# Optimization experiments

Hardware: AMD Instinct MI355X
Metric: run time of the kernel (lower is better)

The kernel has to match this reference:

```python
import jax, jax.numpy as jnp
import numpy as np

D_MODEL = 1024
N_HEAD = 16
D_HEAD = D_MODEL // N_HEAD


def setup_inputs() -> dict:
    key = jax.random.key(0)
    k_x, k_wqkv, k_bqkv, k_wp, k_bp = jax.random.split(key, 5)
    B, T = 2, 2048
    bound = 1.0 / np.sqrt(D_MODEL)
    return {
        "x": jax.random.normal(k_x, (B, T, D_MODEL), dtype=jnp.float32),
        "w_qkv": jax.random.uniform(k_wqkv, (D_MODEL, 3 * D_MODEL), jnp.float32, -bound, bound),
        "b_qkv": jax.random.uniform(k_bqkv, (3 * D_MODEL,), jnp.float32, -bound, bound),
        "w_proj": jax.random.uniform(k_wp, (D_MODEL, D_MODEL), jnp.float32, -bound, bound),
        "b_proj": jax.random.uniform(k_bp, (D_MODEL,), jnp.float32, -bound, bound),
    }


def reference(x, w_qkv, b_qkv, w_proj, b_proj):
    B, T, C = x.shape
    qkv = x @ w_qkv + b_qkv                       # [B,T,3C]
    qkv = qkv.reshape(B, T, 3, N_HEAD, D_HEAD)
    qkv = jnp.transpose(qkv, (2, 0, 3, 1, 4))      # [3,B,H,T,dh]
    q, k, v = qkv[0], qkv[1], qkv[2]
    scale = np.sqrt(D_HEAD).astype(np.float32)
    attn = jnp.einsum("bhqd,bhkd->bhqk", q, k) / scale  # [B,H,T,T]
    causal = jnp.tril(jnp.ones((T, T), dtype=bool))
    attn = jnp.where(causal, attn, -jnp.inf)
    attn = jax.nn.softmax(attn, axis=-1)
    out = jnp.einsum("bhqk,bhkd->bhqd", attn, v)   # [B,H,T,dh]
    out = jnp.transpose(out, (0, 2, 1, 3)).reshape(B, T, C)
    return out @ w_proj + b_proj
```

## Files before the change

kernel.cpp:

```cpp
#include <hip/hip_runtime.h>
#include <hip/hip_bf16.h>
#include <math.h>

constexpr int Bb   = 2;
constexpr int T    = 2048;
constexpr int C    = 1024;
constexpr int H    = 16;
constexpr int M    = Bb * T;
constexpr int NQKV = 3 * C;

typedef __attribute__((ext_vector_type(8))) short bf16x8;
typedef __attribute__((ext_vector_type(4))) float f32x4;

__device__ inline short f2bf(float f) {
    __hip_bfloat16 h = __float2bfloat16(f);
    return *reinterpret_cast<short*>(&h);
}

#if __has_builtin(__builtin_amdgcn_exp2f)
#define EXP2(x) __builtin_amdgcn_exp2f(x)
#else
#define EXP2(x) exp2f(x)
#endif

#define GLOBAL_AS __attribute__((address_space(1)))
#define LDS_AS    __attribute__((address_space(3)))

__device__ __forceinline__ void gload_lds16(const short* g, short* s) {
    __builtin_amdgcn_global_load_lds((const GLOBAL_AS void*)g, (LDS_AS void*)s, 16, 0, 0);
}

__global__ __launch_bounds__(256)
void prep_all(const float* __restrict__ x, short* __restrict__ xb,
              const float* __restrict__ w_qkv, short* __restrict__ wqkvt,
              const float* __restrict__ w_proj, short* __restrict__ wprojt)
{
    __shared__ float tile[32][33];
    const int blk = blockIdx.x;
    const int tid = threadIdx.x;

    if (blk < 4096) {
        const int i = blk * 1024 + tid * 4;
        const float4 v = *(const float4*)(x + i);
        short4 s;
        s.x = f2bf(v.x); s.y = f2bf(v.y); s.z = f2bf(v.z); s.w = f2bf(v.w);
        *(short4*)(xb + i) = s;
        return;
    }

    const bool isqkv = (blk < 7168);
    const int bidx = isqkv ? (blk - 4096) : (blk - 7168);
    const int nblk = isqkv ? 96 : 32;
    const int N    = isqkv ? NQKV : C;
    const float* W = isqkv ? w_qkv : w_proj;
    short* Wt      = isqkv ? wqkvt : wprojt;

    const int n0 = (bidx % nblk) * 32, k0 = (bidx / nblk) * 32;
    const int tx = tid & 31, ty = tid >> 5;
#pragma unroll
    for (int i = 0; i < 32; i += 8)
        tile[ty + i][tx] = W[(size_t)(k0 + ty + i) * N + n0 + tx];
    __syncthreads();
#pragma unroll
    for (int i = 0; i < 32; i += 8)
        Wt[(size_t)(n0 + ty + i) * C + k0 + tx] = f2bf(tile[tx][ty + i]);
}

__global__ __launch_bounds__(256)
void gemm_mfma(const short* __restrict__ A, const short* __restrict__ Bt,
               const float* __restrict__ bias, short* __restrict__ outp,
               int Ndim, int Kdim)
{
    __shared__ __align__(16) short As[2 * 128 * 32];
    __shared__ __align__(16) short Bs[2 * 128 * 32];

    const int tid = threadIdx.x;
    const int w   = tid >> 6;
    const int l   = tid & 63;
    const int lk  = l & 15;
    const int lq  = l >> 4;

    const int gx  = gridDim.x;
    const int nwg = gx * gridDim.y;
    const int cpx = nwg >> 3;
    const int bid = blockIdx.y * gx + blockIdx.x;
    const int swz = (bid & 7) * cpx + (bid >> 3);
    const int m0  = (swz / gx) * 128;
    const int n0  = (swz % gx) * 128;

    const int mw  = (w >> 1) * 64, nw = (w & 1) * 64;

    const int srow = w * 16 + (l >> 2);
    const int scol = (l & 3) * 8;

    const short* agp0 = A  + (size_t)(m0 + srow)      * Kdim + scol;
    const short* agp1 = A  + (size_t)(m0 + 64 + srow) * Kdim + scol;
    const short* bgp0 = Bt + (size_t)(n0 + srow)      * Kdim + scol;
    const short* bgp1 = Bt + (size_t)(n0 + 64 + srow) * Kdim + scol;

    short* ad0 = &As[w * 512];
    short* ad1 = &As[2048 + w * 512];
    short* bd0 = &Bs[w * 512];
    short* bd1 = &Bs[2048 + w * 512];

    f32x4 acc[4][4];
#pragma unroll
    for (int i = 0; i < 4; ++i)
#pragma unroll
        for (int j = 0; j < 4; ++j) acc[i][j] = (f32x4){0.f, 0.f, 0.f, 0.f};

    gload_lds16(agp0, ad0);
    gload_lds16(agp1, ad1);
    gload_lds16(bgp0, bd0);
    gload_lds16(bgp1, bd1);
    __syncthreads();

    int cur = 0;
    for (int k0 = 0; k0 < Kdim; k0 += 32) {
        const int coff = cur ? 4096 : 0;

        if (k0 + 32 < Kdim) {
            const int noff = cur ? 0 : 4096;
            gload_lds16(agp0 + k0 + 32, ad0 + noff);
            gload_lds16(agp1 + k0 + 32, ad1 + noff);
            gload_lds16(bgp0 + k0 + 32, bd0 + noff);
            gload_lds16(bgp1 + k0 + 32, bd1 + noff);
        }

        bf16x8 af[4], bfr[4];
#pragma unroll
        for (int mt = 0; mt < 4; ++mt)
            af[mt] = *(const bf16x8*)&As[coff + (mw + mt * 16 + lk) * 32 + lq * 8];
#pragma unroll
        for (int nt = 0; nt < 4; ++nt)
            bfr[nt] = *(const bf16x8*)&Bs[coff + (nw + nt * 16 + lk) * 32 + lq * 8];

#pragma unroll
        for (int mt = 0; mt < 4; ++mt)
#pragma unroll
            for (int nt = 0; nt < 4; ++nt)
                acc[mt][nt] = __builtin_amdgcn_mfma_f32_16x16x32_bf16(bfr[nt], af[mt], acc[mt][nt], 0, 0, 0);

        __syncthreads();
        cur ^= 1;
    }

    float4 bv[4];
#pragma unroll
    for (int nt = 0; nt < 4; ++nt)
        bv[nt] = *(const float4*)(bias + n0 + nw + nt * 16 + lq * 4);
#pragma unroll
    for (int mt = 0; mt < 4; ++mt) {
        short* rowp = outp + (size_t)(m0 + mw + mt * 16 + lk) * Ndim + n0 + nw + lq * 4;
#pragma unroll
        for (int nt = 0; nt < 4; ++nt) {
            short4 pk;
            pk.x = f2bf(acc[mt][nt][0] + bv[nt].x);
            pk.y = f2bf(acc[mt][nt][1] + bv[nt].y);
            pk.z = f2bf(acc[mt][nt][2] + bv[nt].z);
            pk.w = f2bf(acc[mt][nt][3] + bv[nt].w);
            *(short4*)(rowp + nt * 16) = pk;
        }
    }
}

__global__ __launch_bounds__(256)
void gemm_mfma_proj(const short* __restrict__ A, const short* __restrict__ Bt,
                    const float* __restrict__ bias, float* __restrict__ outp,
                    int Ndim, int Kdim)
{
    __shared__ __align__(16) short As[2 * 64 * 32];
    __shared__ __align__(16) short Bs[2 * 128 * 32];

    const int tid = threadIdx.x;
    const int w   = tid >> 6;
    const int l   = tid & 63;
    const int lk  = l & 15;
    const int lq  = l >> 4;

    const int gx  = gridDim.x;
    const int nwg = gx * gridDim.y;
    const int cpx = nwg >> 3;
    const int bid = blockIdx.y * gx + blockIdx.x;
    const int swz = (bid & 7) * cpx + (bid >> 3);
    const int m0  = (swz / gx) * 64;
    const int n0  = (swz % gx) * 128;

    const int mw  = (w & 1) * 32, nw = (w >> 1) * 64;

    const int srow = w * 16 + (l >> 2);
    const int scol = (l & 3) * 8;

    const short* agp  = A  + (size_t)(m0 + srow)      * Kdim + scol;
    const short* bgp0 = Bt + (size_t)(n0 + srow)      * Kdim + scol;
    const short* bgp1 = Bt + (size_t)(n0 + 64 + srow) * Kdim + scol;

    short* ad  = &As[w * 512];
    short* bd0 = &Bs[w * 512];
    short* bd1 = &Bs[2048 + w * 512];

    f32x4 acc[2][4];
#pragma unroll
    for (int i = 0; i < 2; ++i)
#pragma unroll
        for (int j = 0; j < 4; ++j) acc[i][j] = (f32x4){0.f, 0.f, 0.f, 0.f};

    gload_lds16(agp,  ad);
    gload_lds16(bgp0, bd0);
    gload_lds16(bgp1, bd1);
    __syncthreads();

    int cur = 0;
    for (int k0 = 0; k0 < Kdim; k0 += 32) {
        const int coffA = cur ? 2048 : 0;
        const int coffB = cur ? 4096 : 0;

        if (k0 + 32 < Kdim) {
            const int noffA = cur ? 0 : 2048;
            const int noffB = cur ? 0 : 4096;
            gload_lds16(agp  + k0 + 32, ad  + noffA);
            gload_lds16(bgp0 + k0 + 32, bd0 + noffB);
            gload_lds16(bgp1 + k0 + 32, bd1 + noffB);
        }

        bf16x8 af[2], bfr[4];
#pragma unroll
        for (int mt = 0; mt < 2; ++mt)
            af[mt] = *(const bf16x8*)&As[coffA + (mw + mt * 16 + lk) * 32 + lq * 8];
#pragma unroll
        for (int nt = 0; nt < 4; ++nt)
            bfr[nt] = *(const bf16x8*)&Bs[coffB + (nw + nt * 16 + lk) * 32 + lq * 8];

#pragma unroll
        for (int mt = 0; mt < 2; ++mt)
#pragma unroll
            for (int nt = 0; nt < 4; ++nt)
                acc[mt][nt] = __builtin_amdgcn_mfma_f32_16x16x32_bf16(bfr[nt], af[mt], acc[mt][nt], 0, 0, 0);

        __syncthreads();
        cur ^= 1;
    }

    float4 bv[4];
#pragma unroll
    for (int nt = 0; nt < 4; ++nt)
        bv[nt] = *(const float4*)(bias + n0 + nw + nt * 16 + lq * 4);
#pragma unroll
    for (int mt = 0; mt < 2; ++mt) {
        float* rowp = outp + (size_t)(m0 + mw + mt * 16 + lk) * Ndim + n0 + nw + lq * 4;
#pragma unroll
        for (int nt = 0; nt < 4; ++nt) {
            float4 v;
            v.x = acc[mt][nt][0] + bv[nt].x;
            v.y = acc[mt][nt][1] + bv[nt].y;
            v.z = acc[mt][nt][2] + bv[nt].z;
            v.w = acc[mt][nt][3] + bv[nt].w;
            *(float4*)(rowp + nt * 16) = v;
        }
    }
}

constexpr int LDV = 136;
constexpr float SC = 0.18033688f;
constexpr float M0 = 16.0f;

__global__ __launch_bounds__(512, 2)
void attn_mfma(const short* __restrict__ qkv, short* __restrict__ att)
{
    __shared__ __align__(16) short Ks[2][128 * 64];
    __shared__ __align__(16) short Vt[2][64 * LDV];

    const int idx = blockIdx.x;
    const int xcd = idx & 7;
    const int j   = idx >> 3;
    const int bh  = xcd * 4 + (j & 3);
    const int s   = j >> 2;
    const int qt  = (s < 8) ? s : (23 - s);
    const int b   = bh >> 4;
    const int h   = bh & 15;
    const int qbase = qt * 128;

    const int tid = threadIdx.x;
    const int w   = tid >> 6;
    const int l   = tid & 63;
    const int lk  = l & 15;
    const int lq  = l >> 4;

    const short* base = qkv + (size_t)b * T * 3072 + h * 64;

    const int q_abs = qbase + w * 16 + lk;
    const short* qp = base + (size_t)q_abs * 3072 + lq * 8;
    const bf16x8 qf0 = *(const bf16x8*)qp;
    const bf16x8 qf1 = *(const bf16x8*)(qp + 32);

    f32x4 acc_o[4];
#pragma unroll
    for (int dt = 0; dt < 4; ++dt) acc_o[dt] = (f32x4){0.f, 0.f, 0.f, 0.f};
    float lacc = 0.f;

    const int krow   = l >> 3;
    const int kcolsw = 8 * ((l & 7) ^ (l >> 3));
    const int swz    = lk & 7;

    const int kg   = tid & 31;
    const int vd0  = ((tid >> 5) & 7) * 8;
    const int pcol = ((kg & 24) | ((kg & 3) << 1) | ((kg >> 2) & 1)) * 4;

    const int nkt = qt + 1;

    bf16x8 vv[4];

    if (w < 4) {
#pragma unroll
        for (int rr = 0; rr < 4; ++rr) {
            const int g = w * 32 + rr * 8;
            gload_lds16(base + 1024 + (size_t)(g + krow) * 3072 + kcolsw, &Ks[0][g * 64]);
        }
    } else {
        const short* vp = base + 2048 + (size_t)(kg * 4) * 3072 + vd0;
#pragma unroll
        for (int kk = 0; kk < 4; ++kk)
            vv[kk] = *(const bf16x8*)(vp + (size_t)kk * 3072);
#pragma unroll
        for (int d = 0; d < 8; ++d) {
            short4 pk;
            pk.x = vv[0][d]; pk.y = vv[1][d]; pk.z = vv[2][d]; pk.w = vv[3][d];
            *(short4*)&Vt[0][(vd0 + d) * LDV + pcol] = pk;
        }
    }
    __syncthreads();

#pragma unroll 1
    for (int it = 0; it < nkt; ++it) {
        const int j0  = it * 128;
        const int buf = it & 1;
        const int nb  = buf ^ 1;

        if (it + 1 < nkt) {
            const int j1 = j0 + 128;
            if (w < 4) {
#pragma unroll
                for (int rr = 0; rr < 4; ++rr) {
                    const int g = w * 32 + rr * 8;
                    gload_lds16(base + 1024 + (size_t)(j1 + g + krow) * 3072 + kcolsw,
                                &Ks[nb][g * 64]);
                }
            } else {
                const short* vp = base + 2048 + (size_t)(j1 + kg * 4) * 3072 + vd0;
#pragma unroll
                for (int kk = 0; kk < 4; ++kk)
                    vv[kk] = *(const bf16x8*)(vp + (size_t)kk * 3072);
            }
        }

        f32x4 s4[8];
        __builtin_amdgcn_s_setprio(1);
#pragma unroll
        for (int kt = 0; kt < 8; ++kt) {
            const int row = kt * 16 + lk;
            const bf16x8 kf0 = *(const bf16x8*)&Ks[buf][row * 64 + 8 * (lq ^ swz)];
            const bf16x8 kf1 = *(const bf16x8*)&Ks[buf][row * 64 + 8 * ((lq + 4) ^ swz)];
            f32x4 a = (f32x4){0.f, 0.f, 0.f, 0.f};
            a = __builtin_amdgcn_mfma_f32_16x16x32_bf16(kf0, qf0, a, 0, 0, 0);
            a = __builtin_amdgcn_mfma_f32_16x16x32_bf16(kf1, qf1, a, 0, 0, 0);
            s4[kt] = a;
        }
        __builtin_amdgcn_s_setprio(0);

        if (it == nkt - 1) {
#pragma unroll
            for (int kt = 0; kt < 8; ++kt)
#pragma unroll
                for (int r = 0; r < 4; ++r)
                    if (j0 + kt * 16 + lq * 4 + r > q_abs) s4[kt][r] = -1e30f;
        }

#pragma unroll
        for (int kt = 0; kt < 8; ++kt)
#pragma unroll
            for (int r = 0; r < 4; ++r)
                s4[kt][r] = EXP2(fmaf(s4[kt][r], SC, -M0));

        float ts[8];
#pragma unroll
        for (int kt = 0; kt < 8; ++kt)
            ts[kt] = (s4[kt][0] + s4[kt][1]) + (s4[kt][2] + s4[kt][3]);
        lacc += ((ts[0] + ts[1]) + (ts[2] + ts[3]))
              + ((ts[4] + ts[5]) + (ts[6] + ts[7]));

        unsigned int d0[8], d1[8];
#pragma unroll
        for (int kt = 0; kt < 8; ++kt) {
            d0[kt] = (unsigned int)(unsigned short)f2bf(s4[kt][0])
                   | ((unsigned int)(unsigned short)f2bf(s4[kt][1]) << 16);
            d1[kt] = (unsigned int)(unsigned short)f2bf(s4[kt][2])
                   | ((unsigned int)(unsigned short)f2bf(s4[kt][3]) << 16);
        }

        __builtin_amdgcn_s_setprio(1);
#pragma unroll
        for (int kc = 0; kc < 4; ++kc) {
            union { unsigned int u[4]; bf16x8 v; } up;
            up.u[0] = d0[kc * 2];
            up.u[1] = d1[kc * 2];
            up.u[2] = d0[kc * 2 + 1];
            up.u[3] = d1[kc * 2 + 1];
            const bf16x8 pf = up.v;
#pragma unroll
            for (int dt = 0; dt < 4; ++dt) {
                const bf16x8 vf = *(const bf16x8*)&Vt[buf][(dt * 16 + lk) * LDV + kc * 32 + lq * 8];
                acc_o[dt] = __builtin_amdgcn_mfma_f32_16x16x32_bf16(vf, pf, acc_o[dt], 0, 0, 0);
            }
        }
        __builtin_amdgcn_s_setprio(0);

        if (it + 1 < nkt && w >= 4) {
#pragma unroll
            for (int d = 0; d < 8; ++d) {
                short4 pk;
                pk.x = vv[0][d]; pk.y = vv[1][d]; pk.z = vv[2][d]; pk.w = vv[3][d];
                *(short4*)&Vt[nb][(vd0 + d) * LDV + pcol] = pk;
            }
        }

        __syncthreads();
    }

    float ls = lacc;
    ls += __shfl_xor(ls, 16);
    ls += __shfl_xor(ls, 32);
    const float inv = 1.f / ls;
    short* op = att + ((size_t)(b * T + q_abs)) * 1024 + h * 64;
#pragma unroll
    for (int dt = 0; dt < 4; ++dt) {
        short4 pk;
        pk.x = f2bf(acc_o[dt][0] * inv);
        pk.y = f2bf(acc_o[dt][1] * inv);
        pk.z = f2bf(acc_o[dt][2] * inv);
        pk.w = f2bf(acc_o[dt][3] * inv);
        *(short4*)(op + dt * 16 + lq * 4) = pk;
    }
}

extern "C" void kernel_launch(void* const* d_in, const int* in_sizes, int n_in,
                              void* d_out, int out_size, void* d_ws, size_t ws_size,
                              hipStream_t stream)
{
    const float* x      = (const float*)d_in[0];
    const float* w_qkv  = (const float*)d_in[1];
    const float* b_qkv  = (const float*)d_in[2];
    const float* w_proj = (const float*)d_in[3];
    const float* b_proj = (const float*)d_in[4];
    float* out = (float*)d_out;

    short* xb     = (short*)d_ws;
    short* wqkvt  = xb     + (size_t)M * C;
    short* wprojt = wqkvt  + (size_t)NQKV * C;
    short* qkvb   = wprojt + (size_t)C * C;
    short* attb   = qkvb   + (size_t)M * NQKV;

    prep_all<<<8192, 256, 0, stream>>>(x, xb, w_qkv, wqkvt, w_proj, wprojt);
    gemm_mfma<<<dim3(NQKV / 128, M / 128), 256, 0, stream>>>(xb, wqkvt, b_qkv, qkvb, NQKV, C);
    attn_mfma<<<512, 512, 0, stream>>>(qkvb, attb);
    gemm_mfma_proj<<<dim3(C / 128, M / 64), 256, 0, stream>>>(attb, wprojt, b_proj, out, C, C);
}
```

Measured before the change: 176.7 us.

## Software-pipeline QK^T one tile ahead in attention and hoist GEMM LDS reads

The attention loop now computes the QK^T scores for the next key tile while it runs softmax and PV on the current one, prefetching K and V two tiles ahead into the freed buffers. The aim is to overlap MFMA score work with the exp and convert work and hide global load latency. In both GEMMs, the LDS fragment reads are moved ahead of the async global-to-LDS prefetch issue. Launch bounds for attention rise from 2 to 4 blocks per CU, which caps registers at the same moment the extra s4_next array raises register pressure, so spilling is a risk.

```diff
diff --git a/kernel.cpp b/kernel.cpp
--- a/kernel.cpp
+++ b/kernel.cpp
@@ -119,6 +119,14 @@
     for (int k0 = 0; k0 < Kdim; k0 += 32) {
         const int coff = cur ? 4096 : 0;
 
+        bf16x8 af[4], bfr[4];
+#pragma unroll
+        for (int mt = 0; mt < 4; ++mt)
+            af[mt] = *(const bf16x8*)&As[coff + (mw + mt * 16 + lk) * 32 + lq * 8];
+#pragma unroll
+        for (int nt = 0; nt < 4; ++nt)
+            bfr[nt] = *(const bf16x8*)&Bs[coff + (nw + nt * 16 + lk) * 32 + lq * 8];
+
         if (k0 + 32 < Kdim) {
             const int noff = cur ? 0 : 4096;
             gload_lds16(agp0 + k0 + 32, ad0 + noff);
@@ -126,14 +134,6 @@
             gload_lds16(bgp0 + k0 + 32, bd0 + noff);
             gload_lds16(bgp1 + k0 + 32, bd1 + noff);
         }
-
-        bf16x8 af[4], bfr[4];
-#pragma unroll
-        for (int mt = 0; mt < 4; ++mt)
-            af[mt] = *(const bf16x8*)&As[coff + (mw + mt * 16 + lk) * 32 + lq * 8];
-#pragma unroll
-        for (int nt = 0; nt < 4; ++nt)
-            bfr[nt] = *(const bf16x8*)&Bs[coff + (nw + nt * 16 + lk) * 32 + lq * 8];
 
 #pragma unroll
         for (int mt = 0; mt < 4; ++mt)
@@ -215,6 +215,14 @@
         const int coffA = cur ? 2048 : 0;
         const int coffB = cur ? 4096 : 0;
 
+        bf16x8 af[2], bfr[4];
+#pragma unroll
+        for (int mt = 0; mt < 2; ++mt)
+            af[mt] = *(const bf16x8*)&As[coffA + (mw + mt * 16 + lk) * 32 + lq * 8];
+#pragma unroll
+        for (int nt = 0; nt < 4; ++nt)
+            bfr[nt] = *(const bf16x8*)&Bs[coffB + (nw + nt * 16 + lk) * 32 + lq * 8];
+
         if (k0 + 32 < Kdim) {
             const int noffA = cur ? 0 : 2048;
             const int noffB = cur ? 0 : 4096;
@@ -222,14 +230,6 @@
             gload_lds16(bgp0 + k0 + 32, bd0 + noffB);
             gload_lds16(bgp1 + k0 + 32, bd1 + noffB);
         }
-
-        bf16x8 af[2], bfr[4];
-#pragma unroll
-        for (int mt = 0; mt < 2; ++mt)
-            af[mt] = *(const bf16x8*)&As[coffA + (mw + mt * 16 + lk) * 32 + lq * 8];
-#pragma unroll
-        for (int nt = 0; nt < 4; ++nt)
-            bfr[nt] = *(const bf16x8*)&Bs[coffB + (nw + nt * 16 + lk) * 32 + lq * 8];
 
 #pragma unroll
         for (int mt = 0; mt < 2; ++mt)
@@ -264,7 +264,23 @@
 constexpr float SC = 0.18033688f;
 constexpr float M0 = 16.0f;
 
-__global__ __launch_bounds__(512, 2)
+__device__ __forceinline__ void qk_tile(const short* Kbuf, const bf16x8 qf0,
+                                        const bf16x8 qf1, int lk, int lq, int swz,
+                                        f32x4 s4[8])
+{
+#pragma unroll
+    for (int kt = 0; kt < 8; ++kt) {
+        const int row = kt * 16 + lk;
+        const bf16x8 kf0 = *(const bf16x8*)&Kbuf[row * 64 + 8 * (lq ^ swz)];
+        const bf16x8 kf1 = *(const bf16x8*)&Kbuf[row * 64 + 8 * ((lq + 4) ^ swz)];
+        f32x4 a = (f32x4){0.f, 0.f, 0.f, 0.f};
+        a = __builtin_amdgcn_mfma_f32_16x16x32_bf16(kf0, qf0, a, 0, 0, 0);
+        a = __builtin_amdgcn_mfma_f32_16x16x32_bf16(kf1, qf1, a, 0, 0, 0);
+        s4[kt] = a;
+    }
+}
+
+__global__ __launch_bounds__(512, 4)
 void attn_mfma(const short* __restrict__ qkv, short* __restrict__ att)
 {
     __shared__ __align__(16) short Ks[2][128 * 64];
@@ -330,71 +346,77 @@
     }
     __syncthreads();
 
+    f32x4 s4_cur[8], s4_next[8];
+    __builtin_amdgcn_s_setprio(1);
+    qk_tile(&Ks[0][0], qf0, qf1, lk, lq, swz, s4_cur);
+    __builtin_amdgcn_s_setprio(0);
+
+    if (nkt > 1) {
+        if (w < 4) {
+#pragma unroll
+            for (int rr = 0; rr < 4; ++rr) {
+                const int g = w * 32 + rr * 8;
+                gload_lds16(base + 1024 + (size_t)(128 + g + krow) * 3072 + kcolsw,
+                            &Ks[1][g * 64]);
+            }
+        } else {
+            const short* vp = base + 2048 + (size_t)(128 + kg * 4) * 3072 + vd0;
+#pragma unroll
+            for (int kk = 0; kk < 4; ++kk)
+                vv[kk] = *(const bf16x8*)(vp + (size_t)kk * 3072);
+        }
+    }
+    __syncthreads();
+
 #pragma unroll 1
-    for (int it = 0; it < nkt; ++it) {
-        const int j0  = it * 128;
-        const int buf = it & 1;
-        const int nb  = buf ^ 1;
-
-        if (it + 1 < nkt) {
-            const int j1 = j0 + 128;
-            if (w < 4) {
-#pragma unroll
-                for (int rr = 0; rr < 4; ++rr) {
-                    const int g = w * 32 + rr * 8;
-                    gload_lds16(base + 1024 + (size_t)(j1 + g + krow) * 3072 + kcolsw,
-                                &Ks[nb][g * 64]);
-                }
-            } else {
-                const short* vp = base + 2048 + (size_t)(j1 + kg * 4) * 3072 + vd0;
-#pragma unroll
-                for (int kk = 0; kk < 4; ++kk)
-                    vv[kk] = *(const bf16x8*)(vp + (size_t)kk * 3072);
+    for (int t = 0; t < nkt; ++t) {
+        const int buf = t & 1;
+
+        if (t + 2 < nkt && w < 4) {
+            const int j2 = (t + 2) * 128;
+#pragma unroll
+            for (int rr = 0; rr < 4; ++rr) {
+                const int g = w * 32 + rr * 8;
+                gload_lds16(base + 1024 + (size_t)(j2 + g + krow) * 3072 + kcolsw,
+                            &Ks[buf][g * 64]);
             }
         }
 
-        f32x4 s4[8];
-        __builtin_amdgcn_s_setprio(1);
-#pragma unroll
-        for (int kt = 0; kt < 8; ++kt) {
-            const int row = kt * 16 + lk;
-            const bf16x8 kf0 = *(const bf16x8*)&Ks[buf][row * 64 + 8 * (lq ^ swz)];
-            const bf16x8 kf1 = *(const bf16x8*)&Ks[buf][row * 64 + 8 * ((lq + 4) ^ swz)];
-            f32x4 a = (f32x4){0.f, 0.f, 0.f, 0.f};
-            a = __builtin_amdgcn_mfma_f32_16x16x32_bf16(kf0, qf0, a, 0, 0, 0);
-            a = __builtin_amdgcn_mfma_f32_16x16x32_bf16(kf1, qf1, a, 0, 0, 0);
-            s4[kt] = a;
-        }
-        __builtin_amdgcn_s_setprio(0);
-
-        if (it == nkt - 1) {
+        if (t + 1 < nkt) {
+            __builtin_amdgcn_s_setprio(1);
+            qk_tile(&Ks[buf ^ 1][0], qf0, qf1, lk, lq, swz, s4_next);
+            __builtin_amdgcn_s_setprio(0);
+        }
+
+        if (t == nkt - 1) {
+            const int j0 = t * 128;
 #pragma unroll
             for (int kt = 0; kt < 8; ++kt)
 #pragma unroll
                 for (int r = 0; r < 4; ++r)
-                    if (j0 + kt * 16 + lq * 4 + r > q_abs) s4[kt][r] = -1e30f;
+                    if (j0 + kt * 16 + lq * 4 + r > q_abs) s4_cur[kt][r] = -1e30f;
         }
 
 #pragma unroll
         for (int kt = 0; kt < 8; ++kt)
 #pragma unroll
             for (int r = 0; r < 4; ++r)
-                s4[kt][r] = EXP2(fmaf(s4[kt][r], SC, -M0));
+                s4_cur[kt][r] = EXP2(fmaf(s4_cur[kt][r], SC, -M0));
 
         float ts[8];
 #pragma unroll
         for (int kt = 0; kt < 8; ++kt)
-            ts[kt] = (s4[kt][0] + s4[kt][1]) + (s4[kt][2] + s4[kt][3]);
+            ts[kt] = (s4_cur[kt][0] + s4_cur[kt][1]) + (s4_cur[kt][2] + s4_cur[kt][3]);
         lacc += ((ts[0] + ts[1]) + (ts[2] + ts[3]))
               + ((ts[4] + ts[5]) + (ts[6] + ts[7]));
 
         unsigned int d0[8], d1[8];
 #pragma unroll
         for (int kt = 0; kt < 8; ++kt) {
-            d0[kt] = (unsigned int)(unsigned short)f2bf(s4[kt][0])
-                   | ((unsigned int)(unsigned short)f2bf(s4[kt][1]) << 16);
-            d1[kt] = (unsigned int)(unsigned short)f2bf(s4[kt][2])
-                   | ((unsigned int)(unsigned short)f2bf(s4[kt][3]) << 16);
+            d0[kt] = (unsigned int)(unsigned short)f2bf(s4_cur[kt][0])
+                   | ((unsigned int)(unsigned short)f2bf(s4_cur[kt][1]) << 16);
+            d1[kt] = (unsigned int)(unsigned short)f2bf(s4_cur[kt][2])
+                   | ((unsigned int)(unsigned short)f2bf(s4_cur[kt][3]) << 16);
         }
 
         __builtin_amdgcn_s_setprio(1);
@@ -414,16 +436,27 @@
         }
         __builtin_amdgcn_s_setprio(0);
 
-        if (it + 1 < nkt && w >= 4) {
+        if (t + 1 < nkt && w >= 4) {
 #pragma unroll
             for (int d = 0; d < 8; ++d) {
                 short4 pk;
                 pk.x = vv[0][d]; pk.y = vv[1][d]; pk.z = vv[2][d]; pk.w = vv[3][d];
-                *(short4*)&Vt[nb][(vd0 + d) * LDV + pcol] = pk;
+                *(short4*)&Vt[buf ^ 1][(vd0 + d) * LDV + pcol] = pk;
             }
+            if (t + 2 < nkt) {
+                const short* vp = base + 2048 + (size_t)((t + 2) * 128 + kg * 4) * 3072 + vd0;
+#pragma unroll
+                for (int kk = 0; kk < 4; ++kk)
+                    vv[kk] = *(const bf16x8*)(vp + (size_t)kk * 3072);
+            }
         }
 
         __syncthreads();
+
+        if (t + 1 < nkt) {
+#pragma unroll
+            for (int kt = 0; kt < 8; ++kt) s4_cur[kt] = s4_next[kt];
+        }
     }
 
     float ls = lacc;
```

Measured after the change: 196.4 us. 1.11x slower.

## Rewrite QKV GEMM with 256x256 tiles, XOR-swizzled LDS and phased MFMA pipeline

Applied to the files above, without the earlier changes.

Replaces the 128x128, 4-wave QKV GEMM with a 256x256, 8-wave kernel. It uses BK=64, XOR-swizzled LDS layout, staggered global-to-LDS prefetch across four phases with explicit vmcnt waits and raw s_barrier, and s_setprio around MFMA bursts. The larger tile is meant to raise operand reuse and hide load latency. The cost is much more LDS (128KB per block), higher register pressure, and only 192 blocks for the whole grid. Separately, the projection GEMM now reads LDS fragments before issuing the next prefetch.

```diff
diff --git a/kernel.cpp b/kernel.cpp
--- a/kernel.cpp
+++ b/kernel.cpp
@@ -66,92 +66,106 @@
         Wt[(size_t)(n0 + ty + i) * C + k0 + tx] = f2bf(tile[tx][ty + i]);
 }
 
-__global__ __launch_bounds__(256)
-void gemm_mfma(const short* __restrict__ A, const short* __restrict__ Bt,
-               const float* __restrict__ bias, short* __restrict__ outp,
-               int Ndim, int Kdim)
+__global__ __launch_bounds__(512, 2)
+void gemm_qkv_8ph(const short* __restrict__ A, const short* __restrict__ Bt,
+                  const float* __restrict__ bias, short* __restrict__ outp,
+                  int Ndim, int Kdim)
 {
-    __shared__ __align__(16) short As[2 * 128 * 32];
-    __shared__ __align__(16) short Bs[2 * 128 * 32];
+    __shared__ __align__(16) short As[2][256 * 64];
+    __shared__ __align__(16) short Bs[2][256 * 64];
 
     const int tid = threadIdx.x;
     const int w   = tid >> 6;
     const int l   = tid & 63;
     const int lk  = l & 15;
     const int lq  = l >> 4;
+    const int wm  = w >> 2;
+    const int wn  = w & 3;
 
     const int gx  = gridDim.x;
     const int nwg = gx * gridDim.y;
     const int cpx = nwg >> 3;
     const int bid = blockIdx.y * gx + blockIdx.x;
     const int swz = (bid & 7) * cpx + (bid >> 3);
-    const int m0  = (swz / gx) * 128;
-    const int n0  = (swz % gx) * 128;
-
-    const int mw  = (w >> 1) * 64, nw = (w & 1) * 64;
-
-    const int srow = w * 16 + (l >> 2);
-    const int scol = (l & 3) * 8;
-
-    const short* agp0 = A  + (size_t)(m0 + srow)      * Kdim + scol;
-    const short* agp1 = A  + (size_t)(m0 + 64 + srow) * Kdim + scol;
-    const short* bgp0 = Bt + (size_t)(n0 + srow)      * Kdim + scol;
-    const short* bgp1 = Bt + (size_t)(n0 + 64 + srow) * Kdim + scol;
-
-    short* ad0 = &As[w * 512];
-    short* ad1 = &As[2048 + w * 512];
-    short* bd0 = &Bs[w * 512];
-    short* bd1 = &Bs[2048 + w * 512];
-
-    f32x4 acc[4][4];
-#pragma unroll
-    for (int i = 0; i < 4; ++i)
-#pragma unroll
-        for (int j = 0; j < 4; ++j) acc[i][j] = (f32x4){0.f, 0.f, 0.f, 0.f};
-
-    gload_lds16(agp0, ad0);
-    gload_lds16(agp1, ad1);
-    gload_lds16(bgp0, bd0);
-    gload_lds16(bgp1, bd1);
-    __syncthreads();
-
-    int cur = 0;
-    for (int k0 = 0; k0 < Kdim; k0 += 32) {
-        const int coff = cur ? 4096 : 0;
-
-        if (k0 + 32 < Kdim) {
-            const int noff = cur ? 0 : 4096;
-            gload_lds16(agp0 + k0 + 32, ad0 + noff);
-            gload_lds16(agp1 + k0 + 32, ad1 + noff);
-            gload_lds16(bgp0 + k0 + 32, bd0 + noff);
-            gload_lds16(bgp1 + k0 + 32, bd1 + noff);
-        }
-
-        bf16x8 af[4], bfr[4];
-#pragma unroll
-        for (int mt = 0; mt < 4; ++mt)
-            af[mt] = *(const bf16x8*)&As[coff + (mw + mt * 16 + lk) * 32 + lq * 8];
-#pragma unroll
-        for (int nt = 0; nt < 4; ++nt)
-            bfr[nt] = *(const bf16x8*)&Bs[coff + (nw + nt * 16 + lk) * 32 + lq * 8];
-
-#pragma unroll
-        for (int mt = 0; mt < 4; ++mt)
-#pragma unroll
-            for (int nt = 0; nt < 4; ++nt)
-                acc[mt][nt] = __builtin_amdgcn_mfma_f32_16x16x32_bf16(bfr[nt], af[mt], acc[mt][nt], 0, 0, 0);
-
-        __syncthreads();
-        cur ^= 1;
+    const int m0  = (swz / gx) * 256;
+    const int n0  = (swz % gx) * 256;
+
+    const int srow = l >> 3;
+    const int scol = 8 * ((l & 7) ^ srow);
+    const short* aS = A  + (size_t)(m0 + srow) * Kdim + scol;
+    const short* bS = Bt + (size_t)(n0 + srow) * Kdim + scol;
+
+    const int rsw = lk & 7;
+
+    f32x4 acc[8][4];
+#pragma unroll
+    for (int i = 0; i < 8; ++i)
+#pragma unroll
+        for (int j2 = 0; j2 < 4; ++j2) acc[i][j2] = (f32x4){0.f, 0.f, 0.f, 0.f};
+
+    const int nkt = Kdim >> 6;
+
+#pragma unroll
+    for (int p = 0; p < 4; ++p) {
+        const int g = w * 32 + p * 8;
+        gload_lds16(aS + (size_t)g * Kdim, &As[0][g * 64]);
+        gload_lds16(bS + (size_t)g * Kdim, &Bs[0][g * 64]);
+    }
+
+#pragma unroll 1
+    for (int t = 0; t < nkt; ++t) {
+        const int buf = t & 1;
+        const int nb  = buf ^ 1;
+        const int kn  = (t + 1) << 6;
+
+        bf16x8 af[8];
+#pragma unroll
+        for (int p = 0; p < 4; ++p) {
+            const int kh = p >> 1;
+            const int nh = p & 1;
+
+            if (t + 1 < nkt) {
+                const int g = w * 32 + p * 8;
+                gload_lds16(aS + (size_t)g * Kdim + kn, &As[nb][g * 64]);
+                gload_lds16(bS + (size_t)g * Kdim + kn, &Bs[nb][g * 64]);
+            }
+            if (p == 0) {
+                if (t + 1 < nkt) asm volatile("s_waitcnt vmcnt(2)" ::: "memory");
+                else             asm volatile("s_waitcnt vmcnt(0)" ::: "memory");
+                __builtin_amdgcn_sched_barrier(0);
+            }
+            asm volatile("s_barrier" ::: "memory");
+
+            if (nh == 0) {
+#pragma unroll
+                for (int mt = 0; mt < 8; ++mt)
+                    af[mt] = *(const bf16x8*)&As[buf][(wm * 128 + mt * 16 + lk) * 64
+                                                     + 8 * (((kh << 2) + lq) ^ rsw)];
+            }
+            const bf16x8 bf0 = *(const bf16x8*)&Bs[buf][(wn * 64 + nh * 32 + 0  + lk) * 64
+                                                        + 8 * (((kh << 2) + lq) ^ rsw)];
+            const bf16x8 bf1 = *(const bf16x8*)&Bs[buf][(wn * 64 + nh * 32 + 16 + lk) * 64
+                                                        + 8 * (((kh << 2) + lq) ^ rsw)];
+
+            __builtin_amdgcn_s_setprio(1);
+#pragma unroll
+            for (int mt = 0; mt < 8; ++mt) {
+                acc[mt][nh * 2 + 0] = __builtin_amdgcn_mfma_f32_16x16x32_bf16(bf0, af[mt], acc[mt][nh * 2 + 0], 0, 0, 0);
+                acc[mt][nh * 2 + 1] = __builtin_amdgcn_mfma_f32_16x16x32_bf16(bf1, af[mt], acc[mt][nh * 2 + 1], 0, 0, 0);
+            }
+            __builtin_amdgcn_s_setprio(0);
+        }
+
+        asm volatile("s_barrier" ::: "memory");
     }
 
     float4 bv[4];
 #pragma unroll
     for (int nt = 0; nt < 4; ++nt)
-        bv[nt] = *(const float4*)(bias + n0 + nw + nt * 16 + lq * 4);
-#pragma unroll
-    for (int mt = 0; mt < 4; ++mt) {
-        short* rowp = outp + (size_t)(m0 + mw + mt * 16 + lk) * Ndim + n0 + nw + lq * 4;
+        bv[nt] = *(const float4*)(bias + n0 + wn * 64 + nt * 16 + lq * 4);
+#pragma unroll
+    for (int mt = 0; mt < 8; ++mt) {
+        short* rowp = outp + (size_t)(m0 + wm * 128 + mt * 16 + lk) * Ndim + n0 + wn * 64 + lq * 4;
 #pragma unroll
         for (int nt = 0; nt < 4; ++nt) {
             short4 pk;
@@ -215,6 +229,14 @@
         const int coffA = cur ? 2048 : 0;
         const int coffB = cur ? 4096 : 0;
 
+        bf16x8 af[2], bfr[4];
+#pragma unroll
+        for (int mt = 0; mt < 2; ++mt)
+            af[mt] = *(const bf16x8*)&As[coffA + (mw + mt * 16 + lk) * 32 + lq * 8];
+#pragma unroll
+        for (int nt = 0; nt < 4; ++nt)
+            bfr[nt] = *(const bf16x8*)&Bs[coffB + (nw + nt * 16 + lk) * 32 + lq * 8];
+
         if (k0 + 32 < Kdim) {
             const int noffA = cur ? 0 : 2048;
             const int noffB = cur ? 0 : 4096;
@@ -222,14 +244,6 @@
             gload_lds16(bgp0 + k0 + 32, bd0 + noffB);
             gload_lds16(bgp1 + k0 + 32, bd1 + noffB);
         }
-
-        bf16x8 af[2], bfr[4];
-#pragma unroll
-        for (int mt = 0; mt < 2; ++mt)
-            af[mt] = *(const bf16x8*)&As[coffA + (mw + mt * 16 + lk) * 32 + lq * 8];
-#pragma unroll
-        for (int nt = 0; nt < 4; ++nt)
-            bfr[nt] = *(const bf16x8*)&Bs[coffB + (nw + nt * 16 + lk) * 32 + lq * 8];
 
 #pragma unroll
         for (int mt = 0; mt < 2; ++mt)
@@ -460,7 +474,7 @@
     short* attb   = qkvb   + (size_t)M * NQKV;
 
     prep_all<<<8192, 256, 0, stream>>>(x, xb, w_qkv, wqkvt, w_proj, wprojt);
-    gemm_mfma<<<dim3(NQKV / 128, M / 128), 256, 0, stream>>>(xb, wqkvt, b_qkv, qkvb, NQKV, C);
+    gemm_qkv_8ph<<<dim3(NQKV / 256, M / 256), 512, 0, stream>>>(xb, wqkvt, b_qkv, qkvb, NQKV, C);
     attn_mfma<<<512, 512, 0, stream>>>(qkvb, attb);
     gemm_mfma_proj<<<dim3(C / 128, M / 64), 256, 0, stream>>>(attb, wprojt, b_proj, out, C, C);
 }
```

Result: slower. 187.5 us (+6.1%).
